# Performance work log

Hardware: AMD Instinct MI355X
Metric: run time of the kernel (lower is better)

## Reference

```python
import jax, jax.numpy as jnp
import numpy as np

EPS = 1e-8
TEMP = 0.1
D, H = 512, 256  # hidden_dim, hidden_dim // 2
BI, R = 64, 36   # images, regions
BC, W = 64, 50   # captions, words


def _l2norm(x):
    n = jnp.linalg.norm(x, axis=-1, keepdims=True)
    return x / jnp.maximum(n, 1e-12)


def _gate(x, w1, b1, w2, b2):
    h = jax.nn.relu(x @ w1 + b1)
    return jax.nn.sigmoid(h @ w2 + b2)  # [..., 1]


def setup_inputs() -> dict:
    key = jax.random.key(0)
    ks = jax.random.split(key, 12)
    imgs = jax.random.normal(ks[0], (BI, R, D), dtype=jnp.float32)
    caps = jax.random.normal(ks[1], (BC, W, D), dtype=jnp.float32)
    img_lens = jax.random.randint(ks[2], (BI,), 1, R + 1).at[0].set(R).astype(jnp.int32)
    cap_lens = jax.random.randint(ks[3], (BC,), 1, W + 1).at[0].set(W).astype(jnp.int32)
    s = 0.02
    return {
        'imgs': imgs, 'caps': caps,
        'soft_w1': jax.random.normal(ks[4], (D, H), dtype=jnp.float32) * s,
        'soft_b1': jnp.zeros((H,), dtype=jnp.float32),
        'soft_w2': jax.random.normal(ks[5], (H, 1), dtype=jnp.float32) * s,
        'soft_b2': jnp.zeros((1,), dtype=jnp.float32),
        'hard_w1': jax.random.normal(ks[6], (D, H), dtype=jnp.float32) * s,
        'hard_b1': jnp.zeros((H,), dtype=jnp.float32),
        'hard_w2': jax.random.normal(ks[7], (H, 1), dtype=jnp.float32) * s,
        'hard_b2': jnp.zeros((1,), dtype=jnp.float32),
        'img_lens': img_lens, 'cap_lens': cap_lens,
    }


def reference(imgs, caps, soft_w1, soft_b1, soft_w2, soft_b2,
              hard_w1, hard_b1, hard_w2, hard_b2, img_lens, cap_lens):
    Bi, R_, D_ = imgs.shape
    Bc, W_, _ = caps.shape
    img_mask = jnp.arange(R_)[None, :] < img_lens[:, None]  # [Bi,R]
    cap_mask = jnp.arange(W_)[None, :] < cap_lens[:, None]  # [Bc,W]
    mask = img_mask[:, None, :, None] & cap_mask[None, :, None, :]  # [Bi,Bc,R,W]

    # fine-grained region-word similarities
    sims = jnp.einsum('ird,cwd->icrw', imgs, caps)

    # hard (top-1) attention: argmax over words, one-hot scatter, re-masked
    idx = jnp.argmax(jnp.where(mask, sims, -1.0), axis=-1)  # [Bi,Bc,R]
    hard_attn = jnp.where(mask, jax.nn.one_hot(idx, W_, dtype=sims.dtype), 0.0)

    # soft attention with temperature and mask
    soft = jax.nn.softmax(jnp.where(mask, sims / TEMP, -jnp.inf), axis=-1)
    soft_attn = jnp.where(mask, soft, 0.0)

    hard_wc = jnp.einsum('icrw,cwd->icrd', hard_attn, caps)
    soft_wc = jnp.einsum('icrw,cwd->icrd', soft_attn, caps)

    # per-region learned gates, normalized to sum ~1
    sg = _gate(imgs, soft_w1, soft_b1, soft_w2, soft_b2)  # [Bi,R,1]
    hg = _gate(imgs, hard_w1, hard_b1, hard_w2, hard_b2)  # [Bi,R,1]
    tot = sg + hg + EPS
    sg = (sg / tot)[:, None, :, :]  # [Bi,1,R,1]
    hg = (hg / tot)[:, None, :, :]

    mixed = sg * soft_wc + hg * hard_wc  # [Bi,Bc,R,D]

    # per-pair, per-region cosine similarity
    out = jnp.einsum('ird,icrd->icr', _l2norm(imgs), _l2norm(mixed))
    return jnp.where(img_mask[:, None, :], out, -1.0)  # [Bi,Bc,R]
```

## Files before the change

### kernel.cpp

```cpp
#include <hip/hip_runtime.h>
#include <math.h>

#define BI 64
#define RR 36
#define BC 64
#define WW 50
#define DD 512
#define HH 256
#define CST 132

typedef _Float16 f16x8 __attribute__((ext_vector_type(8)));
typedef _Float16 f16x4 __attribute__((ext_vector_type(4)));
typedef float    f32x4 __attribute__((ext_vector_type(4)));
typedef float    f32x16 __attribute__((ext_vector_type(16)));

__device__ __forceinline__ float wave_sum(float v){
  #pragma unroll
  for (int off=32; off>0; off>>=1) v += __shfl_xor(v, off, 64);
  return v;
}
__device__ __forceinline__ float wave_max(float v){
  #pragma unroll
  for (int off=32; off>0; off>>=1) v = fmaxf(v, __shfl_xor(v, off, 64));
  return v;
}

__global__ __launch_bounds__(256, 2) void sgemm_hgate_kernel(
    const float* __restrict__ imgs, const float* __restrict__ caps,
    const float* __restrict__ sw1, const float* __restrict__ hw1,
    const float* __restrict__ sb1, const float* __restrict__ hb1,
    const float* __restrict__ sw2, const float* __restrict__ hw2,
    float* __restrict__ Sp,
    float* __restrict__ drawS, float* __restrict__ drawH,
    float* __restrict__ rnraw,
    float* __restrict__ G, _Float16* __restrict__ Gfrag)
{
  __shared__ __align__(16) _Float16 lds[2*16384];
  const int t = threadIdx.x, lane = t & 63, wv = t >> 6;

  if (blockIdx.x >= 36 && blockIdx.x < 486){
    const int sg  = blockIdx.x - 36;
    const int xcd = sg & 7, sidx = sg >> 3;
    const int l   = (xcd < 2 ? xcd*57 : 114 + (xcd-2)*56) + sidx;
    const int st  = l / 45, wi = l - st*45;
    const int mbg = st & 1, nbg = st >> 1;
    const int mb  = mbg*9 + wi/5;
    const int nb  = nbg*5 + wi%5;
    const int wm = wv & 1, wn = wv >> 1;

    f32x4 P[4][4], Q[4][4];
    #pragma unroll
    for (int a=0;a<4;a++)
      #pragma unroll
      for (int b=0;b<4;b++){ P[a][b]=(f32x4){0,0,0,0}; Q[a][b]=(f32x4){0,0,0,0}; }

    const float* srcb = (wv < 2) ? imgs : caps;
    const int tb   = ((wv<2)? mb : nb)*8 + (wv&1)*4;
    const int mrow = lane & 15;
    const int kq   = (lane >> 4)*8;
    const float* sp0 = srcb + ((size_t)(tb*16 + mrow))*DD + kq;
    const int regoff = ((wv<2)? 0 : 8192) + ((wv&1)*4)*512 + lane*8;

    float4 va[4], vb[4];
    auto sg_load = [&](int ks){
      #pragma unroll
      for (int s=0;s<4;s++){
        const float* p = sp0 + (size_t)s*16*DD + ks*32;
        va[s] = *(const float4*)p;
        vb[s] = *(const float4*)(p+4);
      }
    };
    auto sg_write = [&](int bufi){
      _Float16* Lh = lds + bufi*16384 + regoff;
      #pragma unroll
      for (int s=0;s<4;s++){
        float e[8] = {va[s].x,va[s].y,va[s].z,va[s].w,
                      vb[s].x,vb[s].y,vb[s].z,vb[s].w};
        f16x8 hv, lv;
        #pragma unroll
        for (int j=0;j<8;j++){
          _Float16 h = (_Float16)e[j];
          hv[j] = h;
          lv[j] = (_Float16)((e[j]-(float)h)*2048.0f);
        }
        *(f16x8*)&Lh[s*512]        = hv;
        *(f16x8*)&Lh[4096 + s*512] = lv;
      }
    };

    sg_load(0); sg_write(0);
    __syncthreads();

    for (int ks=0; ks<16; ks++){
      if (ks < 15) sg_load(ks+1);

      const _Float16* L = lds + (ks & 1)*16384;
      f16x8 a_h[4], a_l[4], b_h[4], b_l[4];
      #pragma unroll
      for (int x=0;x<4;x++){
        a_h[x] = *(const f16x8*)&L[        (wm*4+x)*512 + lane*8];
        a_l[x] = *(const f16x8*)&L[ 4096 + (wm*4+x)*512 + lane*8];
        b_h[x] = *(const f16x8*)&L[ 8192 + (wn*4+x)*512 + lane*8];
        b_l[x] = *(const f16x8*)&L[12288 + (wn*4+x)*512 + lane*8];
      }
      #pragma unroll
      for (int mi=0;mi<4;mi++)
        #pragma unroll
        for (int ni=0;ni<4;ni++){
          P[mi][ni] = __builtin_amdgcn_mfma_f32_16x16x32_f16(a_h[mi], b_h[ni], P[mi][ni],0,0,0);
          Q[mi][ni] = __builtin_amdgcn_mfma_f32_16x16x32_f16(a_h[mi], b_l[ni], Q[mi][ni],0,0,0);
          Q[mi][ni] = __builtin_amdgcn_mfma_f32_16x16x32_f16(a_l[mi], b_h[ni], Q[mi][ni],0,0,0);
        }

      if (ks < 15) sg_write((ks+1)&1);
      __syncthreads();
    }

    const int r0 = mb*128 + wm*64 + ((lane>>4)<<2);
    const int c0 = nb*128 + wn*64 + (lane&15);
    size_t pr[16]; size_t pc[4];
    #pragma unroll
    for (int mi=0;mi<4;mi++)
      #pragma unroll
      for (int reg=0;reg<4;reg++){
        unsigned row = (unsigned)(r0 + mi*16 + reg);
        unsigned i = row / 36u, rr_ = row - i*36u;
        pr[mi*4+reg] = (size_t)i*115200u + (size_t)rr_*50u;
      }
    #pragma unroll
    for (int ni=0;ni<4;ni++){
      unsigned col = (unsigned)(c0 + ni*16);
      unsigned cc = col / 50u, w = col - cc*50u;
      pc[ni] = (size_t)cc*1800u + w;
    }
    #pragma unroll
    for (int mi=0;mi<4;mi++)
      #pragma unroll
      for (int ni=0;ni<4;ni++)
        #pragma unroll
        for (int reg=0;reg<4;reg++)
          Sp[pr[mi*4+reg] + pc[ni]] =
              P[mi][ni][reg] + Q[mi][ni][reg]*(1.0f/2048.0f);
    return;
  }

  if (blockIdx.x >= 486){
    float* Gt = (float*)lds;
    const int c = blockIdx.x - 486;
    const int wm = wv & 1, wn = wv >> 1;
    const float* cbase = caps + (size_t)c*WW*DD;

    f32x16 P, Q;
    #pragma unroll
    for (int e=0;e<16;e++){ P[e]=0.f; Q[e]=0.f; }

    const int r  = lane & 31;
    const int k8 = (lane >> 5)*8;
    const int wA = wm*32 + r;
    const int wB = wn*32 + r;
    const float* pA = cbase + (size_t)wA*DD + k8;
    const float* pB = cbase + (size_t)wB*DD + k8;

    for (int ks=0; ks<32; ks++){
      const int k0 = ks*16;
      float4 a0, a1, b0, b1;
      if (wA < WW){ a0 = *(const float4*)(pA + k0); a1 = *(const float4*)(pA + k0 + 4); }
      else        { a0 = (float4){0,0,0,0}; a1 = a0; }
      if (wB < WW){ b0 = *(const float4*)(pB + k0); b1 = *(const float4*)(pB + k0 + 4); }
      else        { b0 = (float4){0,0,0,0}; b1 = b0; }
      float av[8] = {a0.x,a0.y,a0.z,a0.w,a1.x,a1.y,a1.z,a1.w};
      float bw[8] = {b0.x,b0.y,b0.z,b0.w,b1.x,b1.y,b1.z,b1.w};
      f16x8 ah, al, bh, bl;
      #pragma unroll
      for (int j=0;j<8;j++){
        _Float16 h = (_Float16)av[j];
        ah[j] = h; al[j] = (_Float16)((av[j]-(float)h)*2048.0f);
        _Float16 g = (_Float16)bw[j];
        bh[j] = g; bl[j] = (_Float16)((bw[j]-(float)g)*2048.0f);
      }
      P = __builtin_amdgcn_mfma_f32_32x32x16_f16(ah, bh, P,0,0,0);
      Q = __builtin_amdgcn_mfma_f32_32x32x16_f16(ah, bl, Q,0,0,0);
      Q = __builtin_amdgcn_mfma_f32_32x32x16_f16(al, bh, Q,0,0,0);
    }

    const int col = wn*32 + (lane & 31);
    #pragma unroll
    for (int reg=0; reg<16; reg++){
      const int row = wm*32 + (reg&3) + 8*(reg>>2) + 4*(lane>>5);
      float g = P[reg] + Q[reg]*(1.0f/2048.0f);
      Gt[row*64 + col] = g;
      if (row < WW && col < WW)
        G[(size_t)c*WW*WW + row*WW + col] = g;
    }
    __syncthreads();

    #pragma unroll
    for (int tile=0; tile<4; tile++){
      int flat = t*4;
      int ks2 = flat>>9, L=(flat>>3)&63, j0=flat&7;
      const bool ones = (tile==3) && ((L&15)==2);
      int n  = tile*16 + (L&15);
      int kk = ks2*32 + ((L>>4)<<3) + j0;
      f16x4 v;
      #pragma unroll
      for (int e=0;e<4;e++)
        v[e] = ones ? (_Float16)1.0f : (_Float16)Gt[n*64 + kk + e];
      *(f16x4*)&Gfrag[(size_t)c*4096 + (tile*2+ks2)*512 + L*8 + j0] = v;
    }
    return;
  }

  const int mb = blockIdx.x >> 1;
  const int br = blockIdx.x & 1;
  const int wm = wv & 1, wn = wv >> 1;
  const float* W = br ? hw1 : sw1;

  f32x4 P[4][8];
  #pragma unroll
  for (int a=0;a<4;a++)
    #pragma unroll
    for (int b=0;b<8;b++) P[a][b]=(f32x4){0,0,0,0};

  const int mrow = lane & 15, kq = (lane>>4)*8;
  const float* apA = imgs + ((size_t)((mb*8 + wv*2)*16 + mrow))*DD + kq;
  const int nb0 = (wv*4)*16 + mrow;

  float4 va[2][2];
  float wreg[4][8];
  auto hg_load = [&](int ks){
    #pragma unroll
    for (int s=0;s<2;s++){
      const float* p = apA + (size_t)s*16*DD + ks*32;
      va[s][0] = *(const float4*)p;
      va[s][1] = *(const float4*)(p+4);
    }
    #pragma unroll
    for (int sb=0;sb<4;sb++){
      const float* q = W + (size_t)(ks*32 + kq)*HH + (nb0 + sb*16);
      #pragma unroll
      for (int j=0;j<8;j++) wreg[sb][j] = q[(size_t)j*HH];
    }
  };
  auto hg_write = [&](int bufi){
    _Float16* buf = lds + bufi*16384;
    #pragma unroll
    for (int s=0;s<2;s++){
      float e[8] = {va[s][0].x,va[s][0].y,va[s][0].z,va[s][0].w,
                    va[s][1].x,va[s][1].y,va[s][1].z,va[s][1].w};
      f16x8 hv;
      #pragma unroll
      for (int j=0;j<8;j++) hv[j] = (_Float16)e[j];
      *(f16x8*)&buf[(wv*2+s)*512 + lane*8] = hv;
    }
    #pragma unroll
    for (int sb=0;sb<4;sb++){
      f16x8 hv;
      #pragma unroll
      for (int j=0;j<8;j++) hv[j] = (_Float16)wreg[sb][j];
      *(f16x8*)&buf[4096 + (wv*4+sb)*512 + lane*8] = hv;
    }
  };

  hg_load(0); hg_write(0);
  __syncthreads();

  for (int ks=0; ks<16; ks++){
    if (ks < 15) hg_load(ks+1);

    const _Float16* L = lds + (ks & 1)*16384;
    f16x8 a[4], b[8];
    #pragma unroll
    for (int x=0;x<4;x++)
      a[x] = *(const f16x8*)&L[(wm*4+x)*512 + lane*8];
    #pragma unroll
    for (int y=0;y<8;y++)
      b[y] = *(const f16x8*)&L[4096 + (wn*8+y)*512 + lane*8];
    #pragma unroll
    for (int mi=0;mi<4;mi++)
      #pragma unroll
      for (int ni=0;ni<8;ni++)
        P[mi][ni] = __builtin_amdgcn_mfma_f32_16x16x32_f16(a[mi], b[ni], P[mi][ni],0,0,0);

    if (ks < 15) hg_write((ks+1)&1);
    __syncthreads();
  }

  const float* b1 = br ? hb1 : sb1;
  const float* w2 = br ? hw2 : sw2;
  float bvv[8], wvv[8];
  #pragma unroll
  for (int ni=0;ni<8;ni++){
    const int cb = wn*128 + ni*16 + (lane&15);
    bvv[ni] = b1[cb]; wvv[ni] = w2[cb];
  }
  float contrib[16];
  #pragma unroll
  for (int mi=0;mi<4;mi++)
    #pragma unroll
    for (int reg=0;reg<4;reg++){
      float cacc = 0.f;
      #pragma unroll
      for (int ni=0;ni<8;ni++)
        cacc = fmaf(fmaxf(P[mi][ni][reg] + bvv[ni], 0.f), wvv[ni], cacc);
      #pragma unroll
      for (int off=1; off<16; off<<=1) cacc += __shfl_xor(cacc, off, 64);
      contrib[mi*4+reg] = cacc;
    }

  float* red = (float*)lds;
  __syncthreads();
  if ((lane & 15) == 0){
    const int rbase = wm*64 + ((lane>>4)<<2);
    #pragma unroll
    for (int mi=0;mi<4;mi++)
      #pragma unroll
      for (int reg=0;reg<4;reg++)
        red[wn*128 + rbase + mi*16 + reg] = contrib[mi*4+reg];
  }
  __syncthreads();
  if (t < 128){
    float draw = red[t] + red[128 + t];
    (br ? drawH : drawS)[mb*128 + t] = draw;
  }

  if (br == 0){
    const int row = mb*128 + (t >> 1);
    const float* p = imgs + (size_t)row*DD + (t & 1)*256;
    float ss = 0.f;
    #pragma unroll
    for (int q=0;q<64;q++){
      float4 x = ((const float4*)p)[q];
      ss += x.x*x.x + x.y*x.y + x.z*x.z + x.w*x.w;
    }
    ss += __shfl_xor(ss, 1, 64);
    if ((t & 1) == 0) rnraw[row] = ss;
  }
}

__global__ __launch_bounds__(256) void epi_kernel(
    const float* __restrict__ Sp,
    const int* __restrict__ img_lens, const int* __restrict__ cap_lens,
    const float* __restrict__ drawS, const float* __restrict__ drawH,
    const float* __restrict__ rnraw,
    const float* __restrict__ G, const _Float16* __restrict__ Gfrag,
    const float* __restrict__ sb2, const float* __restrict__ hb2,
    float* __restrict__ out)
{
  __shared__ __align__(16) _Float16 FT[4][48*72];
  const int t = threadIdx.x, lane = t & 63;
  const int wv = __builtin_amdgcn_readfirstlane(t >> 6);
  const int pair = blockIdx.x*4 + wv;
  const int i = pair >> 6, c = pair & 63;
  const int l = lane & 15, g = lane >> 4;
  const int cap_len = cap_lens[c];
  const int img_len = img_lens[i];

  int4 gf[8];
  #pragma unroll
  for (int q=0;q<8;q++)
    gf[q] = ((const int4*)(Gfrag + (size_t)c*4096))[q*64 + lane];

  const float* sbp = Sp + (size_t)i*115200 + (size_t)c*1800;
  float sv[3][16];
  #pragma unroll
  for (int nt=0;nt<3;nt++)
    #pragma unroll
    for (int ks=0;ks<2;ks++){
      const float* p = sbp + (nt*16+l)*50 + ks*32 + g*8;
      #pragma unroll
      for (int h=0;h<4;h++){
        float2 v2 = *(const float2*)(p + h*2);
        sv[nt][ks*8 + h*2]     = v2.x;
        sv[nt][ks*8 + h*2 + 1] = v2.y;
      }
    }

  float avA[3]; int aiA[3]; float denA[3], tSA[3];
  f16x8 e16[3][2];
  #pragma unroll
  for (int nt=0;nt<3;nt++){
    float best = -INFINITY; int bw = 64;
    #pragma unroll
    for (int j=0;j<16;j++){
      int w = (j>>3)*32 + g*8 + (j&7);
      if (w < cap_len){
        float s = sv[nt][j];
        if (s > best){ best = s; bw = w; }
      }
    }
    #pragma unroll
    for (int off=16; off<64; off<<=1){
      float ov = __shfl_xor(best, off, 64);
      int   ow = __shfl_xor(bw,   off, 64);
      if (ov > best || (ov == best && ow < bw)){ best = ov; bw = ow; }
    }
    avA[nt] = best; aiA[nt] = (bw < 64) ? bw : 0;

    float dsum = 0.f, tsum = 0.f;
    #pragma unroll
    for (int ks=0;ks<2;ks++)
      #pragma unroll
      for (int j=0;j<8;j++){
        int w = ks*32 + g*8 + j;
        float s = sv[nt][ks*8+j];
        float e = (w < cap_len) ? __expf(10.0f*(s - best)) : 0.f;
        _Float16 eh = (_Float16)e;
        e16[nt][ks][j] = eh;
        dsum += (float)eh;
        tsum += (float)(_Float16)(e * s);
      }
    dsum += __shfl_xor(dsum,16,64); dsum += __shfl_xor(dsum,32,64);
    tsum += __shfl_xor(tsum,16,64); tsum += __shfl_xor(tsum,32,64);
    denA[nt] = dsum; tSA[nt] = tsum;
  }

  _Float16* ft = &FT[wv][0];
  #pragma unroll
  for (int mt=0;mt<4;mt++)
    #pragma unroll
    for (int nt=0;nt<3;nt++){
      f32x4 acc = (f32x4){0,0,0,0};
      #pragma unroll
      for (int ks=0;ks<2;ks++){
        f16x8 ga = *(const f16x8*)&gf[mt*2+ks];
        acc = __builtin_amdgcn_mfma_f32_16x16x32_f16(ga, e16[nt][ks], acc,0,0,0);
      }
      f16x4 fv;
      #pragma unroll
      for (int r2=0;r2<4;r2++) fv[r2] = (_Float16)acc[r2];
      *(f16x4*)&ft[(nt*16+l)*72 + mt*16 + g*4] = fv;
    }

  float tQA[3];
  #pragma unroll
  for (int nt=0;nt<3;nt++){
    float q = 0.f;
    #pragma unroll
    for (int ks=0;ks<2;ks++){
      f16x8 fv = *(const f16x8*)&ft[(nt*16+l)*72 + ks*32 + g*8];
      #pragma unroll
      for (int j=0;j<8;j++)
        q += (float)e16[nt][ks][j] * (float)fv[j];
    }
    q += __shfl_xor(q,16,64); q += __shfl_xor(q,32,64);
    tQA[nt] = q;
  }

  if (lane < 16){
    const float sb2v = sb2[0], hb2v = hb2[0];
    #pragma unroll
    for (int nt=0;nt<3;nt++){
      const int rr = nt*16 + lane;
      if (rr < RR){
        const int ai = aiA[nt];
        const float av = avA[nt];
        float dh = (float)ft[rr*72 + ai];
        float hh = G[(size_t)c*WW*WW + ai*(WW+1)];
        float hv = (av > -1.0f) ? 1.f : 0.f;
        const int rg = i*RR + rr;
        float sg_ = 1.f/(1.f+__expf(-(drawS[rg] + sb2v)));
        float hg_ = 1.f/(1.f+__expf(-(drawH[rg] + hb2v)));
        float tot = sg_ + hg_ + 1e-8f;
        float gs = sg_/tot, gh = hg_/tot;
        float rx = 1.f/fmaxf(sqrtf(rnraw[rg]), 1e-12f);
        float dn = (float)(_Float16)denA[nt];
        float rd = 1.f/dn;
        float num = gs*(tSA[nt]*rd) + hv*gh*av;
        float n2  = gs*gs*(tQA[nt]*rd*rd) + hv*(2.f*gs*gh*(dh*rd) + gh*gh*hh);
        float ov  = num * rx / fmaxf(sqrtf(fmaxf(n2, 0.f)), 1e-12f);
        out[((size_t)i*BC + c)*RR + rr] = (rr < img_len) ? ov : -1.0f;
      }
    }
  }
}

__global__ __launch_bounds__(256) void gates_kernel(
    const float* __restrict__ imgs,
    const float* __restrict__ sw1, const float* __restrict__ sb1,
    const float* __restrict__ sw2, const float* __restrict__ sb2,
    const float* __restrict__ hw1, const float* __restrict__ hb1,
    const float* __restrict__ hw2, const float* __restrict__ hb2,
    float* __restrict__ sgn, float* __restrict__ hgn, float* __restrict__ rn)
{
  __shared__ __align__(16) float xs[8*DD];
  __shared__ float red[16*256];
  __shared__ float nr[8];
  const int t = threadIdx.x;
  const int row0 = blockIdx.x * 8;
  if (t < 8) nr[t] = 0.f;
  __syncthreads();
  const float4* src = (const float4*)(imgs + (size_t)row0*DD);
  #pragma unroll
  for (int m=0;m<4;m++){
    int n = m*256+t;
    float4 v = src[n];
    ((float4*)xs)[n] = v;
    float ss = v.x*v.x+v.y*v.y+v.z*v.z+v.w*v.w;
    atomicAdd(&nr[n>>7], ss);
  }
  __syncthreads();
  float accS[8]={0,0,0,0,0,0,0,0};
  float accH[8]={0,0,0,0,0,0,0,0};
  for (int k=0;k<DD;k+=4){
    float a0=sw1[(k+0)*HH+t], a1=sw1[(k+1)*HH+t], a2=sw1[(k+2)*HH+t], a3=sw1[(k+3)*HH+t];
    float b0=hw1[(k+0)*HH+t], b1=hw1[(k+1)*HH+t], b2=hw1[(k+2)*HH+t], b3=hw1[(k+3)*HH+t];
    #pragma unroll
    for (int r=0;r<8;r++){
      float4 x = *(const float4*)&xs[r*DD+k];
      accS[r]=fmaf(x.x,a0,accS[r]); accS[r]=fmaf(x.y,a1,accS[r]);
      accS[r]=fmaf(x.z,a2,accS[r]); accS[r]=fmaf(x.w,a3,accS[r]);
      accH[r]=fmaf(x.x,b0,accH[r]); accH[r]=fmaf(x.y,b1,accH[r]);
      accH[r]=fmaf(x.z,b2,accH[r]); accH[r]=fmaf(x.w,b3,accH[r]);
    }
  }
  const float b1s=sb1[t], b1h=hb1[t], w2s=sw2[t], w2h=hw2[t];
  #pragma unroll
  for (int r=0;r<8;r++){
    red[r*256+t]     = w2s * fmaxf(accS[r]+b1s, 0.f);
    red[(8+r)*256+t] = w2h * fmaxf(accH[r]+b1h, 0.f);
  }
  __syncthreads();
  const int wv=t>>6, ln=t&63;
  #pragma unroll
  for (int q=0;q<4;q++){
    int rr_ = wv*4+q;
    float v = red[rr_*256+ln]+red[rr_*256+ln+64]+red[rr_*256+ln+128]+red[rr_*256+ln+192];
    v = wave_sum(v);
    if (ln==0) red[rr_*256] = v;
  }
  __syncthreads();
  if (t<8){
    float os = red[t*256] + sb2[0];
    float oh = red[(8+t)*256] + hb2[0];
    float s = 1.f/(1.f+__expf(-os));
    float h = 1.f/(1.f+__expf(-oh));
    float tot = s+h+1e-8f;
    sgn[row0+t] = s/tot;
    hgn[row0+t] = h/tot;
    rn[row0+t]  = 1.f/fmaxf(sqrtf(nr[t]), 1e-12f);
  }
}

__global__ __launch_bounds__(256) void gram_fb_kernel(
    const float* __restrict__ caps, float* __restrict__ G)
{
  __shared__ __align__(16) float cs[WW*CST];
  const int c    = blockIdx.x >> 2;
  const int tile = blockIdx.x & 3;
  const int w0   = tile*13;
  const int nw   = (tile==3) ? 11 : 13;
  const int t=threadIdx.x, lane=t&63, wv=t>>6;
  const int wl = lane < WW ? lane : WW-1;
  float acc[4]={0.f,0.f,0.f,0.f};
  for (int k0=0;k0<DD;k0+=128){
    __syncthreads();
    for (int n=t;n<WW*32;n+=256){
      int row=n>>5, c4=(n&31)*4;
      *(float4*)&cs[row*CST+c4] = *(const float4*)(caps + ((size_t)c*WW+row)*DD + k0 + c4);
    }
    __syncthreads();
    for (int k=0;k<128;k+=4){
      float4 cv = *(const float4*)&cs[wl*CST+k];
      #pragma unroll
      for (int q=0;q<4;q++){
        int lw = wv + q*4;
        if (lw < nw){
          float4 bv = *(const float4*)&cs[(w0+lw)*CST+k];
          acc[q]=fmaf(bv.x,cv.x,acc[q]); acc[q]=fmaf(bv.y,cv.y,acc[q]);
          acc[q]=fmaf(bv.z,cv.z,acc[q]); acc[q]=fmaf(bv.w,cv.w,acc[q]);
        }
      }
    }
  }
  if (lane < WW){
    #pragma unroll
    for (int q=0;q<4;q++){
      int lw = wv + q*4;
      if (lw < nw) G[(size_t)c*WW*WW + (w0+lw)*WW + lane] = acc[q];
    }
  }
}

__global__ __launch_bounds__(256) void pair_kernel(
    const float* __restrict__ imgs, const float* __restrict__ caps,
    const int* __restrict__ img_lens, const int* __restrict__ cap_lens,
    const float* __restrict__ sgn, const float* __restrict__ hgn,
    const float* __restrict__ rn,
    const float* __restrict__ G, float* __restrict__ out)
{
  __shared__ __align__(16) float smem[WW*CST + 52*52 + RR*52];
  float* cs = smem;
  float* Gs = smem + WW*CST;
  float* As = Gs + 52*52;
  const int bx = blockIdx.x;
  const int i = bx >> 6, c = bx & 63;
  const int t = threadIdx.x, lane = t&63;
  const int wv = __builtin_amdgcn_readfirstlane(t>>6);
  const int wl = lane < WW ? lane : WW-1;
  const int cap_len = cap_lens[c];
  const int img_len = img_lens[i];
  for (int n=t;n<52*52;n+=256){
    int w=n/52, w2=n-w*52;
    Gs[n] = (w<WW && w2<WW) ? G[(size_t)c*WW*WW + w*WW + w2] : 0.f;
  }
  float acc[9]={0,0,0,0,0,0,0,0,0};
  const float* ib = imgs + ((size_t)i*RR + wv*9)*DD;
  for (int k0=0;k0<DD;k0+=128){
    __syncthreads();
    for (int n=t;n<WW*32;n+=256){
      int row=n>>5, c4=(n&31)*4;
      *(float4*)&cs[row*CST+c4] = *(const float4*)(caps + ((size_t)c*WW+row)*DD + k0 + c4);
    }
    __syncthreads();
    for (int k=0;k<128;k+=4){
      float4 cv = *(const float4*)&cs[wl*CST+k];
      #pragma unroll
      for (int j=0;j<9;j++){
        float4 iv = *(const float4*)(ib + j*DD + k0 + k);
        acc[j]=fmaf(iv.x,cv.x,acc[j]); acc[j]=fmaf(iv.y,cv.y,acc[j]);
        acc[j]=fmaf(iv.z,cv.z,acc[j]); acc[j]=fmaf(iv.w,cv.w,acc[j]);
      }
    }
  }
  for (int j=0;j<9;j++){
    const int r = wv*9 + j;
    const float s = acc[j];
    float av; int ai;
    if (lane < cap_len){ av = s;     ai = lane; }
    else if (lane < WW){ av = -1.0f; ai = lane; }
    else               { av = -INFINITY; ai = 64; }
    #pragma unroll
    for (int off=32; off>0; off>>=1){
      float ov = __shfl_xor(av, off, 64);
      int   oi = __shfl_xor(ai, off, 64);
      if (ov > av || (ov == av && oi < ai)){ av = ov; ai = oi; }
    }
    float zv = (lane < cap_len) ? s*10.0f : -INFINITY;
    float zm = wave_max(zv);
    float e  = (lane < cap_len) ? __expf(zv - zm) : 0.f;
    float den = wave_sum(e);
    if (lane < 52) As[r*52 + lane] = (lane < WW) ? e : 0.f;
    float m = 0.f;
    #pragma unroll
    for (int g=0; g<13; g++){
      float4 ab = *(const float4*)&As[r*52 + g*4];
      m = fmaf(ab.x, Gs[(g*4+0)*52+wl], m);
      m = fmaf(ab.y, Gs[(g*4+1)*52+wl], m);
      m = fmaf(ab.z, Gs[(g*4+2)*52+wl], m);
      m = fmaf(ab.w, Gs[(g*4+3)*52+wl], m);
    }
    float tS = wave_sum(e * s);
    float tQ = wave_sum(e * m);
    float dh = __shfl(m, ai, 64);
    float hh = Gs[ai*52 + ai];
    float hv = (ai < cap_len) ? 1.f : 0.f;
    const int rg = i*RR + r;
    float gs = sgn[rg], gh = hgn[rg], rx = rn[rg];
    float rd = 1.f/den;
    float num = gs*(tS*rd) + hv*gh*av;
    float n2  = gs*gs*(tQ*rd*rd) + hv*(2.f*gs*gh*(dh*rd) + gh*gh*hh);
    float ov  = num * rx / fmaxf(sqrtf(fmaxf(n2, 0.f)), 1e-12f);
    if (lane==0) out[((size_t)i*BC + c)*RR + r] = (r < img_len) ? ov : -1.0f;
  }
}

extern "C" void kernel_launch(void* const* d_in, const int* in_sizes, int n_in,
                              void* d_out, int out_size, void* d_ws, size_t ws_size,
                              hipStream_t stream)
{
  const float* imgs = (const float*)d_in[0];
  const float* caps = (const float*)d_in[1];
  const float* sw1  = (const float*)d_in[2];
  const float* sb1  = (const float*)d_in[3];
  const float* sw2  = (const float*)d_in[4];
  const float* sb2  = (const float*)d_in[5];
  const float* hw1  = (const float*)d_in[6];
  const float* hb1  = (const float*)d_in[7];
  const float* hw2  = (const float*)d_in[8];
  const float* hb2  = (const float*)d_in[9];
  const int* img_lens = (const int*)d_in[10];
  const int* cap_lens = (const int*)d_in[11];

  char* base = (char*)d_ws;
  float*    drawS = (float*)(base + 0);
  float*    drawH = (float*)(base + 9216);
  float*    rnraw = (float*)(base + 18432);
  float*    G     = (float*)(base + 27648);
  _Float16* Gfrag = (_Float16*)(base + 667648);
  float*    Sp    = (float*)(base + 18231296);
  const size_t NEED = 47726592ull;

  float* out = (float*)d_out;

  if (ws_size >= NEED){
    hipLaunchKernelGGL(sgemm_hgate_kernel, dim3(550), dim3(256), 0, stream,
                       imgs, caps, sw1, hw1, sb1, hb1, sw2, hw2,
                       Sp, drawS, drawH, rnraw, G, Gfrag);
    hipLaunchKernelGGL(epi_kernel, dim3(1024), dim3(256), 0, stream,
                       Sp, img_lens, cap_lens, drawS, drawH, rnraw,
                       G, Gfrag, sb2, hb2, out);
  } else {
    hipLaunchKernelGGL(gates_kernel, dim3(288), dim3(256), 0, stream,
                       imgs, sw1, sb1, sw2, sb2, hw1, hb1, hw2, hb2,
                       drawS, drawH, rnraw);
    hipLaunchKernelGGL(gram_fb_kernel, dim3(256), dim3(256), 0, stream, caps, G);
    hipLaunchKernelGGL(pair_kernel, dim3(BI*BC), dim3(256), 0, stream,
                       imgs, caps, img_lens, cap_lens, drawS, drawH, rnraw, G, out);
  }
}
```

Before: 143.6 us.

## Halve sims GEMM tile rows to 64x128 and raise occupancy

The fused sims GEMM blocks now compute 64x128 tiles instead of 128x128, doubling the GEMM block count from 450 to 900 and remapping the XCD-aware tile schedule to match. Each wave loads three 16-row slabs, and shared memory per buffer shrinks, so launch bounds rise to three blocks per CU. The goal is better load balance across CUs and more latency hiding. In exchange, each caps tile is reloaded twice as often and per-tile MFMA reuse drops.

```diff
diff --git a/kernel.cpp b/kernel.cpp
--- a/kernel.cpp
+++ b/kernel.cpp
@@ -25,7 +25,7 @@
   return v;
 }
 
-__global__ __launch_bounds__(256, 2) void sgemm_hgate_kernel(
+__global__ __launch_bounds__(256, 3) void sgemm_hgate_kernel(
     const float* __restrict__ imgs, const float* __restrict__ caps,
     const float* __restrict__ sw1, const float* __restrict__ hw1,
     const float* __restrict__ sb1, const float* __restrict__ hb1,
@@ -35,45 +35,53 @@
     float* __restrict__ rnraw,
     float* __restrict__ G, _Float16* __restrict__ Gfrag)
 {
-  __shared__ __align__(16) _Float16 lds[2*16384];
+  __shared__ __align__(16) _Float16 lds[2*12288];
   const int t = threadIdx.x, lane = t & 63, wv = t >> 6;
 
-  if (blockIdx.x >= 36 && blockIdx.x < 486){
+  if (blockIdx.x >= 36 && blockIdx.x < 936){
     const int sg  = blockIdx.x - 36;
     const int xcd = sg & 7, sidx = sg >> 3;
-    const int l   = (xcd < 2 ? xcd*57 : 114 + (xcd-2)*56) + sidx;
+    const int l   = (xcd < 4 ? xcd*113 : 452 + (xcd-4)*112) + sidx;
     const int st  = l / 45, wi = l - st*45;
-    const int mbg = st & 1, nbg = st >> 1;
-    const int mb  = mbg*9 + wi/5;
-    const int nb  = nbg*5 + wi%5;
+    const int mb  = (st & 3)*9 + wi/5;
+    const int nb  = (st >> 2)*5 + wi%5;
     const int wm = wv & 1, wn = wv >> 1;
 
-    f32x4 P[4][4], Q[4][4];
-    #pragma unroll
-    for (int a=0;a<4;a++)
+    f32x4 P[2][4], Q[2][4];
+    #pragma unroll
+    for (int a=0;a<2;a++)
       #pragma unroll
       for (int b=0;b<4;b++){ P[a][b]=(f32x4){0,0,0,0}; Q[a][b]=(f32x4){0,0,0,0}; }
 
-    const float* srcb = (wv < 2) ? imgs : caps;
-    const int tb   = ((wv<2)? mb : nb)*8 + (wv&1)*4;
-    const int mrow = lane & 15;
-    const int kq   = (lane >> 4)*8;
-    const float* sp0 = srcb + ((size_t)(tb*16 + mrow))*DD + kq;
-    const int regoff = ((wv<2)? 0 : 8192) + ((wv&1)*4)*512 + lane*8;
-
-    float4 va[4], vb[4];
+    const int mrow = lane & 15, kq = (lane>>4)*8;
+    const float* psrc[3]; int hoff[3], loff[3];
+    #pragma unroll
+    for (int s=0;s<3;s++){
+      const int p = wv*3 + s;
+      if (p < 4){
+        psrc[s] = imgs + ((size_t)(mb*64 + p*16 + mrow))*DD + kq;
+        hoff[s] = p*512 + lane*8;
+        loff[s] = 2048 + p*512 + lane*8;
+      } else {
+        psrc[s] = caps + ((size_t)(nb*128 + (p-4)*16 + mrow))*DD + kq;
+        hoff[s] = 4096 + (p-4)*512 + lane*8;
+        loff[s] = 8192 + (p-4)*512 + lane*8;
+      }
+    }
+
+    float4 va[3], vb[3];
     auto sg_load = [&](int ks){
       #pragma unroll
-      for (int s=0;s<4;s++){
-        const float* p = sp0 + (size_t)s*16*DD + ks*32;
+      for (int s=0;s<3;s++){
+        const float* p = psrc[s] + ks*32;
         va[s] = *(const float4*)p;
         vb[s] = *(const float4*)(p+4);
       }
     };
     auto sg_write = [&](int bufi){
-      _Float16* Lh = lds + bufi*16384 + regoff;
-      #pragma unroll
-      for (int s=0;s<4;s++){
+      _Float16* B = lds + bufi*12288;
+      #pragma unroll
+      for (int s=0;s<3;s++){
         float e[8] = {va[s].x,va[s].y,va[s].z,va[s].w,
                       vb[s].x,vb[s].y,vb[s].z,vb[s].w};
         f16x8 hv, lv;
@@ -83,8 +91,8 @@
           hv[j] = h;
           lv[j] = (_Float16)((e[j]-(float)h)*2048.0f);
         }
-        *(f16x8*)&Lh[s*512]        = hv;
-        *(f16x8*)&Lh[4096 + s*512] = lv;
+        *(f16x8*)&B[hoff[s]] = hv;
+        *(f16x8*)&B[loff[s]] = lv;
       }
     };
 
@@ -94,17 +102,20 @@
     for (int ks=0; ks<16; ks++){
       if (ks < 15) sg_load(ks+1);
 
-      const _Float16* L = lds + (ks & 1)*16384;
-      f16x8 a_h[4], a_l[4], b_h[4], b_l[4];
-      #pragma unroll
-      for (int x=0;x<4;x++){
-        a_h[x] = *(const f16x8*)&L[        (wm*4+x)*512 + lane*8];
-        a_l[x] = *(const f16x8*)&L[ 4096 + (wm*4+x)*512 + lane*8];
-        b_h[x] = *(const f16x8*)&L[ 8192 + (wn*4+x)*512 + lane*8];
-        b_l[x] = *(const f16x8*)&L[12288 + (wn*4+x)*512 + lane*8];
-      }
-      #pragma unroll
-      for (int mi=0;mi<4;mi++)
+      const _Float16* L = lds + (ks & 1)*12288;
+      f16x8 a_h[2], a_l[2], b_h[4], b_l[4];
+      #pragma unroll
+      for (int x=0;x<2;x++){
+        a_h[x] = *(const f16x8*)&L[        (wm*2+x)*512 + lane*8];
+        a_l[x] = *(const f16x8*)&L[ 2048 + (wm*2+x)*512 + lane*8];
+      }
+      #pragma unroll
+      for (int y=0;y<4;y++){
+        b_h[y] = *(const f16x8*)&L[ 4096 + (wn*4+y)*512 + lane*8];
+        b_l[y] = *(const f16x8*)&L[ 8192 + (wn*4+y)*512 + lane*8];
+      }
+      #pragma unroll
+      for (int mi=0;mi<2;mi++)
         #pragma unroll
         for (int ni=0;ni<4;ni++){
           P[mi][ni] = __builtin_amdgcn_mfma_f32_16x16x32_f16(a_h[mi], b_h[ni], P[mi][ni],0,0,0);
@@ -116,11 +127,11 @@
       __syncthreads();
     }
 
-    const int r0 = mb*128 + wm*64 + ((lane>>4)<<2);
+    const int r0 = mb*64 + wm*32 + ((lane>>4)<<2);
     const int c0 = nb*128 + wn*64 + (lane&15);
-    size_t pr[16]; size_t pc[4];
-    #pragma unroll
-    for (int mi=0;mi<4;mi++)
+    size_t pr[8]; size_t pc[4];
+    #pragma unroll
+    for (int mi=0;mi<2;mi++)
       #pragma unroll
       for (int reg=0;reg<4;reg++){
         unsigned row = (unsigned)(r0 + mi*16 + reg);
@@ -134,7 +145,7 @@
       pc[ni] = (size_t)cc*1800u + w;
     }
     #pragma unroll
-    for (int mi=0;mi<4;mi++)
+    for (int mi=0;mi<2;mi++)
       #pragma unroll
       for (int ni=0;ni<4;ni++)
         #pragma unroll
@@ -144,9 +155,9 @@
     return;
   }
 
-  if (blockIdx.x >= 486){
+  if (blockIdx.x >= 936){
     float* Gt = (float*)lds;
-    const int c = blockIdx.x - 486;
+    const int c = blockIdx.x - 936;
     const int wm = wv & 1, wn = wv >> 1;
     const float* cbase = caps + (size_t)c*WW*DD;
 
@@ -242,7 +253,7 @@
     }
   };
   auto hg_write = [&](int bufi){
-    _Float16* buf = lds + bufi*16384;
+    _Float16* buf = lds + bufi*12288;
     #pragma unroll
     for (int s=0;s<2;s++){
       float e[8] = {va[s][0].x,va[s][0].y,va[s][0].z,va[s][0].w,
@@ -267,7 +278,7 @@
   for (int ks=0; ks<16; ks++){
     if (ks < 15) hg_load(ks+1);
 
-    const _Float16* L = lds + (ks & 1)*16384;
+    const _Float16* L = lds + (ks & 1)*12288;
     f16x8 a[4], b[8];
     #pragma unroll
     for (int x=0;x<4;x++)
@@ -693,7 +704,7 @@
   float* out = (float*)d_out;
 
   if (ws_size >= NEED){
-    hipLaunchKernelGGL(sgemm_hgate_kernel, dim3(550), dim3(256), 0, stream,
+    hipLaunchKernelGGL(sgemm_hgate_kernel, dim3(1000), dim3(256), 0, stream,
                        imgs, caps, sw1, hw1, sb1, hb1, sw2, hw2,
                        Sp, drawS, drawH, rnraw, G, Gfrag);
     hipLaunchKernelGGL(epi_kernel, dim3(1024), dim3(256), 0, stream,
```

Result: slower. 191.0 us (+33.1%).
